# Performance work log

Hardware: AMD Instinct MI355X
Metric: run time of the kernel (lower is better)

## Reference

```python
import jax, jax.numpy as jnp
import numpy as np

DIM = 128
HEADS = 8
HD = DIM // HEADS          # 16
KS = 8                     # neighborhood kernel size
STRIDE = 2                 # GNA query-group stride
DIL = 2                    # dilation


def axis_indices(L, k, s, d):
    """Per-axis neighborhood indices [L, k] for dilated, strided, edge-clamped NA.

    Queries are grouped in blocks of `s`; every query in a block shares the
    window of the block's center query (GNA 'stride'). Dilation partitions the
    axis into `d` sub-grids; the window lives on the center query's sub-grid
    and is clamped so it never leaves the axis (natten-style sliding window).
    """
    idx = np.zeros((L, k), dtype=np.int32)
    for i in range(L):
        ic = min((i // s) * s + (s - 1) // 2, L - 1)   # group-center query
        r = ic % d                                      # sub-grid (residue)
        Lsub = (L - r + d - 1) // d                     # sub-grid length
        ii = ic // d                                    # index within sub-grid
        start = min(max(ii - (k - 1) // 2, 0), max(Lsub - k, 0))
        for j in range(k):
            idx[i, j] = r + d * min(start + j, Lsub - 1)
    return idx


def setup_inputs() -> dict:
    key = jax.random.key(0)
    ks = jax.random.split(key, 5)
    x = jax.random.normal(ks[0], (1, DIM, 96, 96), jnp.float32)
    # depthwise-grouped qkv conv: Conv2d(dim, 3*dim, 3, 1, 1, groups=dim)
    qkv_w = jax.random.normal(ks[1], (3 * DIM, 1, 3, 3), jnp.float32) * 0.1
    qkv_b = jax.random.normal(ks[2], (3 * DIM,), jnp.float32) * 0.02
    # 1x1 projection: Conv2d(dim, dim, 1)
    proj_w = jax.random.normal(ks[3], (DIM, DIM, 1, 1), jnp.float32) * (DIM ** -0.5)
    proj_b = jax.random.normal(ks[4], (DIM,), jnp.float32) * 0.02
    return {"x": x, "qkv_w": qkv_w, "qkv_b": qkv_b, "proj_w": proj_w, "proj_b": proj_b}


def reference(x, qkv_w, qkv_b, proj_w, proj_b):
    B, C, H, W = x.shape
    # grouped (groups=C) 3x3 conv producing q,k,v
    qkv = jax.lax.conv_general_dilated(
        x, qkv_w, window_strides=(1, 1), padding=[(1, 1), (1, 1)],
        dimension_numbers=("NCHW", "OIHW", "NCHW"), feature_group_count=C)
    qkv = qkv + qkv_b[None, :, None, None]
    qkv = qkv.reshape(B, 3, C, H, W)

    def to_heads(t):  # b c h w -> b h w nh hd
        return t.reshape(B, HEADS, HD, H, W).transpose(0, 3, 4, 1, 2)

    q = to_heads(qkv[:, 0])
    k = to_heads(qkv[:, 1])
    v = to_heads(qkv[:, 2])

    scale = HD ** -0.5
    ri = jnp.asarray(axis_indices(H, KS, STRIDE, DIL))  # [H, KS]
    ci = jnp.asarray(axis_indices(W, KS, STRIDE, DIL))  # [W, KS]
    R = ri[:, :, None, None]       # [H, KS, 1, 1]
    Cc = ci[None, None, :, :]      # [1, 1, W, KS]
    k_win = k[:, R, Cc]            # [B, H, KS, W, KS, nh, hd]
    v_win = v[:, R, Cc]

    logits = jnp.einsum("bijnd,bipjqnd->bijnpq", q * scale, k_win)
    attn = jax.nn.softmax(logits.reshape(B, H, W, HEADS, KS * KS), axis=-1)
    attn = attn.reshape(B, H, W, HEADS, KS, KS)
    out = jnp.einsum("bijnpq,bipjqnd->bijnd", attn, v_win)

    out = out.transpose(0, 3, 4, 1, 2).reshape(B, C, H, W)  # b h w nh hd -> b c h w
    out = jnp.einsum("bchw,oc->bohw", out, proj_w[:, :, 0, 0]) + proj_b[None, :, None, None]
    return out
```

## Files before the change

kernel.cpp:

```cpp
#include <hip/hip_runtime.h>
#include <hip/hip_bf16.h>

#define HH   96
#define WW   96
#define NPIX 9216
#define CH   128
#define NH   8
#define HD   16
#define KS   8

#define NEPIX   2304
#define NPOS    120
#define KVPITCH 40
#define QTPITCH 136
#define KVTPITCH 264
#define XPITCH  97

__device__ __forceinline__ unsigned short f2bf(float f) {
    __hip_bfloat16 b = __float2bfloat16(f);
    union { __hip_bfloat16 b; unsigned short u; } cv; cv.b = b; return cv.u;
}
__device__ __forceinline__ void u4_to_f8(uint4 u, float* f) {
    f[0] = __uint_as_float(u.x << 16); f[1] = __uint_as_float(u.x & 0xffff0000u);
    f[2] = __uint_as_float(u.y << 16); f[3] = __uint_as_float(u.y & 0xffff0000u);
    f[4] = __uint_as_float(u.z << 16); f[5] = __uint_as_float(u.z & 0xffff0000u);
    f[6] = __uint_as_float(u.w << 16); f[7] = __uint_as_float(u.w & 0xffff0000u);
}

__global__ __launch_bounds__(256) void conv_kernel(
    const float* __restrict__ x,
    const float* __restrict__ w,
    const float* __restrict__ bias,
    unsigned short* __restrict__ q_pm,
    unsigned short* __restrict__ kv_pm)
{
    __shared__ float ldsx[128 * XPITCH];
    __shared__ unsigned short qt [24 * QTPITCH];
    __shared__ unsigned short kvt[12 * KVTPITCH];

    const int row = blockIdx.x >> 2;
    const int qtr = blockIdx.x & 3;
    const int j0q = qtr * 24;
    const int tid = threadIdx.x;
    const int g   = tid >> 1;
    const int sh  = tid & 1;
    const bool kvrow = (row & 1) == 0;

    #pragma unroll
    for (int it = 0; it < 12; ++it) {
        const int t  = it * 256 + tid;
        const int r  = t >> 10;
        const int c  = (t >> 3) & 127;
        const int s4 = t & 7;
        const int rg = row + r - 1;
        const int j  = j0q - 4 + s4 * 4;
        float4 v = make_float4(0.f, 0.f, 0.f, 0.f);
        if (rg >= 0 && rg < HH && j >= 0 && j < WW)
            v = *(const float4*)(x + (size_t)c * NPIX + rg * WW + j);
        *(float4*)&ldsx[c * XPITCH + r * 32 + s4 * 4] = v;
    }
    __syncthreads();

    float xr[3][14];
    {
        const float* xg_l = &ldsx[g * XPITCH + 3 + sh * 12];
        #pragma unroll
        for (int dr = 0; dr < 3; ++dr)
            #pragma unroll
            for (int m = 0; m < 14; ++m)
                xr[dr][m] = xg_l[dr * 32 + m];
    }

    #pragma unroll
    for (int dt = 0; dt < 3; ++dt) {
        const int o = 3 * g + dt;
        const int t = o >> 7;
        const int c = o & 127;
        float w9[9];
        #pragma unroll
        for (int k = 0; k < 9; ++k) w9[k] = w[o * 9 + k];
        const float b = bias[o];

        if (t == 0) {
            #pragma unroll
            for (int px = 0; px < 12; ++px) {
                float acc = b;
                #pragma unroll
                for (int kh = 0; kh < 3; ++kh)
                    #pragma unroll
                    for (int kw = 0; kw < 3; ++kw)
                        acc += xr[kh][px + kw] * w9[kh * 3 + kw];
                qt[(sh * 12 + px) * QTPITCH + c] = f2bf(acc);
            }
        } else if (kvrow) {
            #pragma unroll
            for (int pe = 0; pe < 6; ++pe) {
                const int px = pe * 2;
                float acc = b;
                #pragma unroll
                for (int kh = 0; kh < 3; ++kh)
                    #pragma unroll
                    for (int kw = 0; kw < 3; ++kw)
                        acc += xr[kh][px + kw] * w9[kh * 3 + kw];
                kvt[(sh * 6 + pe) * KVTPITCH + (t - 1) * CH + c] = f2bf(acc);
            }
        }
    }

    __syncthreads();

    const int ntask = kvrow ? 768 : 384;
    #pragma unroll
    for (int it = 0; it < 3; ++it) {
        const int idx = it * 256 + tid;
        if (idx < 384) {
            const int px  = idx >> 4;
            const int c8  = (idx & 15) * 8;
            const uint4 v = *(const uint4*)&qt[px * QTPITCH + c8];
            *(uint4*)(q_pm + ((size_t)(row * WW) + j0q + px) * CH + c8) = v;
        } else if (idx < ntask) {
            const int k2  = idx - 384;
            const int epx = k2 >> 5;
            const int c32 = (k2 & 31) * 8;
            const int t1  = c32 >> 7;
            const int c   = c32 & 127;
            const uint4 v = *(const uint4*)&kvt[epx * KVTPITCH + c32];
            *(uint4*)(kv_pm + ((size_t)t1 * NEPIX + (row >> 1) * 48
                               + (j0q >> 1) + epx) * CH + c) = v;
        }
    }
}

__global__ __launch_bounds__(256) void attn_kernel(
    const unsigned short* __restrict__ q_pm,
    const unsigned short* __restrict__ kv_pm,
    float* __restrict__ a_t)
{
    __shared__ unsigned short kv[2][NPOS * KVPITCH];

    const int tid = threadIdx.x;
    const int seg = blockIdx.x;
    const int hp  = blockIdx.y;
    const int i   = seg / 6;
    const int j0  = (seg - i * 6) * 16;
    const int rs     = 2 * min(max(i / 2 - 3, 0), 40);
    const int cs_min = 2 * min(max(j0 / 2 - 3, 0), 40);
    const int er0 = rs >> 1;
    const int ec0 = cs_min >> 1;

    #pragma unroll
    for (int it = 0; it < 4; ++it) {
        const int idx = it * 256 + tid;
        if (idx < 960) {
            const int kvsel = idx / 480;
            const int rem   = idx - kvsel * 480;
            const int pos   = rem >> 2;
            const int sub   = rem & 3;
            const int p     = pos / 15;
            const int cc    = pos - p * 15;
            const int ec    = min(ec0 + cc, 47);
            const int ep    = (er0 + p) * 48 + ec;
            *(uint4*)&kv[kvsel][pos * KVPITCH + sub * 8] =
                *(const uint4*)(kv_pm + ((size_t)kvsel * NEPIX + ep) * CH
                                + hp * 32 + sub * 8);
        }
    }

    const int lane  = tid & 63;
    const int wave  = tid >> 6;
    const int r     = lane >> 3;
    const int hh    = (lane >> 2) & 1;
    const int px    = wave * 4 + (lane & 3);
    const int h     = hp * 2 + hh;
    const int pix   = seg * 16 + px;
    const int j     = j0 + px;
    const int ci0   = (2 * min(max(j / 2 - 3, 0), 40) - cs_min) >> 1;

    float qr[HD];
    {
        const unsigned short* qp = q_pm + (size_t)pix * CH + h * HD;
        u4_to_f8(*(const uint4*)qp, qr);
        u4_to_f8(*(const uint4*)(qp + 8), qr + 8);
        #pragma unroll
        for (int d = 0; d < HD; ++d) qr[d] *= 0.25f;
    }

    __syncthreads();

    const int posr = r * 15 + ci0;
    float lg[KS];
    float m = -1e30f;
    #pragma unroll
    for (int q = 0; q < KS; ++q) {
        const unsigned short* kp = &kv[0][(posr + q) * KVPITCH + hh * HD];
        float kf[HD];
        u4_to_f8(*(const uint4*)kp, kf);
        u4_to_f8(*(const uint4*)(kp + 8), kf + 8);
        float acc = 0.f;
        #pragma unroll
        for (int d = 0; d < HD; ++d) acc += qr[d] * kf[d];
        lg[q] = acc;
        m = fmaxf(m, acc);
    }

    float s = 0.f;
    #pragma unroll
    for (int q = 0; q < KS; ++q) { lg[q] = __expf(lg[q] - m); s += lg[q]; }

    float o[HD];
    #pragma unroll
    for (int d = 0; d < HD; ++d) o[d] = 0.f;
    #pragma unroll
    for (int q = 0; q < KS; ++q) {
        const unsigned short* vp = &kv[1][(posr + q) * KVPITCH + hh * HD];
        float vf[HD];
        u4_to_f8(*(const uint4*)vp, vf);
        u4_to_f8(*(const uint4*)(vp + 8), vf + 8);
        const float wgt = lg[q];
        #pragma unroll
        for (int d = 0; d < HD; ++d) o[d] += wgt * vf[d];
    }

    #pragma unroll
    for (int mask = 8; mask <= 32; mask <<= 1) {
        const float m2 = __shfl_xor(m, mask);
        const float s2 = __shfl_xor(s, mask);
        const float mn = fmaxf(m, m2);
        const float ea = __expf(m - mn);
        const float eb = __expf(m2 - mn);
        s = s * ea + s2 * eb;
        #pragma unroll
        for (int d = 0; d < HD; ++d) {
            const float o2 = __shfl_xor(o[d], mask);
            o[d] = o[d] * ea + o2 * eb;
        }
        m = mn;
    }
    const float inv = 1.f / s;

    a_t[(size_t)(h * HD + 2 * r)     * NPIX + pix] = o[2 * r]     * inv;
    a_t[(size_t)(h * HD + 2 * r + 1) * NPIX + pix] = o[2 * r + 1] * inv;
}

__global__ __launch_bounds__(256) void proj_kernel(
    const float* __restrict__ a_t,
    const float* __restrict__ pw,
    const float* __restrict__ pb,
    float* __restrict__ out)
{
    __shared__ float at[CH][36];

    const int tid = threadIdx.x;
    const int px0 = blockIdx.x * 32;

    #pragma unroll
    for (int it = 0; it < 4; ++it) {
        const int idx = it * 256 + tid;
        const int c   = idx >> 3;
        const int p4  = (idx & 7) * 4;
        *(float4*)&at[c][p4] =
            *(const float4*)(a_t + (size_t)c * NPIX + px0 + p4);
    }
    __syncthreads();

    const int og = tid >> 3;
    const int o0 = og * 4;
    const int p0 = (tid & 7) * 4;

    float acc[4][4];
    #pragma unroll
    for (int i = 0; i < 4; ++i) {
        const float b = pb[o0 + i];
        #pragma unroll
        for (int j = 0; j < 4; ++j) acc[i][j] = b;
    }

    #pragma unroll 2
    for (int c0 = 0; c0 < CH; c0 += 4) {
        float4 wv[4];
        #pragma unroll
        for (int i = 0; i < 4; ++i)
            wv[i] = *(const float4*)(pw + (size_t)(o0 + i) * CH + c0);
        float4 av[4];
        #pragma unroll
        for (int k = 0; k < 4; ++k)
            av[k] = *(const float4*)&at[c0 + k][p0];
        #pragma unroll
        for (int i = 0; i < 4; ++i) {
            acc[i][0] += wv[i].x * av[0].x; acc[i][1] += wv[i].x * av[0].y;
            acc[i][2] += wv[i].x * av[0].z; acc[i][3] += wv[i].x * av[0].w;
            acc[i][0] += wv[i].y * av[1].x; acc[i][1] += wv[i].y * av[1].y;
            acc[i][2] += wv[i].y * av[1].z; acc[i][3] += wv[i].y * av[1].w;
            acc[i][0] += wv[i].z * av[2].x; acc[i][1] += wv[i].z * av[2].y;
            acc[i][2] += wv[i].z * av[2].z; acc[i][3] += wv[i].z * av[2].w;
            acc[i][0] += wv[i].w * av[3].x; acc[i][1] += wv[i].w * av[3].y;
            acc[i][2] += wv[i].w * av[3].z; acc[i][3] += wv[i].w * av[3].w;
        }
    }

    #pragma unroll
    for (int i = 0; i < 4; ++i)
        *(float4*)(out + (size_t)(o0 + i) * NPIX + px0 + p0)
            = make_float4(acc[i][0], acc[i][1], acc[i][2], acc[i][3]);
}

extern "C" void kernel_launch(void* const* d_in, const int* in_sizes, int n_in,
                              void* d_out, int out_size, void* d_ws, size_t ws_size,
                              hipStream_t stream)
{
    const float* x      = (const float*)d_in[0];
    const float* qkv_w  = (const float*)d_in[1];
    const float* qkv_b  = (const float*)d_in[2];
    const float* proj_w = (const float*)d_in[3];
    const float* proj_b = (const float*)d_in[4];
    float* out = (float*)d_out;

    unsigned short* q_pm  = (unsigned short*)d_ws;
    unsigned short* kv_pm = q_pm + (size_t)NPIX * CH;
    float*          a_t   = (float*)(kv_pm + (size_t)2 * NEPIX * CH);

    conv_kernel<<<384, 256, 0, stream>>>(x, qkv_w, qkv_b, q_pm, kv_pm);
    attn_kernel<<<dim3(576, 4), 256, 0, stream>>>(q_pm, kv_pm, a_t);
    proj_kernel<<<288, 256, 0, stream>>>(a_t, proj_w, proj_b, out);
}
```

Baseline: 99.57 us.

## Fuse neighborhood attention and 1x1 projection into one 1024-thread kernel

Merges the attention and projection kernels. Each block now covers all four head pairs for a 16-pixel segment, loads the full 128-channel K/V tile into shared memory once, keeps the attention output in shared memory, and applies the 128x128 projection in place. This removes the a_t round trip through global memory and one kernel launch. In exchange, blocks become much larger with more shared memory, which lowers occupancy. The projection's register tiling is also much smaller, so each thread reads more weights from global or cache.

```diff
diff --git a/kernel.cpp b/kernel.cpp
--- a/kernel.cpp
+++ b/kernel.cpp
@@ -11,10 +11,11 @@
 
 #define NEPIX   2304
 #define NPOS    120
-#define KVPITCH 40
 #define QTPITCH 136
 #define KVTPITCH 264
 #define XPITCH  97
+#define KVP2    136
+#define AOPITCH 132
 
 __device__ __forceinline__ unsigned short f2bf(float f) {
     __hip_bfloat16 b = __float2bfloat16(f);
@@ -131,16 +132,18 @@
     }
 }
 
-__global__ __launch_bounds__(256) void attn_kernel(
+__global__ __launch_bounds__(1024) void attnproj_kernel(
     const unsigned short* __restrict__ q_pm,
     const unsigned short* __restrict__ kv_pm,
-    float* __restrict__ a_t)
+    const float* __restrict__ pw,
+    const float* __restrict__ pb,
+    float* __restrict__ out)
 {
-    __shared__ unsigned short kv[2][NPOS * KVPITCH];
+    __shared__ unsigned short kv[2][NPOS][KVP2];
+    __shared__ float ao[16][AOPITCH];
 
     const int tid = threadIdx.x;
     const int seg = blockIdx.x;
-    const int hp  = blockIdx.y;
     const int i   = seg / 6;
     const int j0  = (seg - i * 6) * 16;
     const int rs     = 2 * min(max(i / 2 - 3, 0), 40);
@@ -150,27 +153,28 @@
 
     #pragma unroll
     for (int it = 0; it < 4; ++it) {
-        const int idx = it * 256 + tid;
-        if (idx < 960) {
-            const int kvsel = idx / 480;
-            const int rem   = idx - kvsel * 480;
-            const int pos   = rem >> 2;
-            const int sub   = rem & 3;
+        const int idx = it * 1024 + tid;
+        if (idx < 3840) {
+            const int kvsel = idx / 1920;
+            const int rem   = idx - kvsel * 1920;
+            const int pos   = rem >> 4;
+            const int c8    = rem & 15;
             const int p     = pos / 15;
             const int cc    = pos - p * 15;
             const int ec    = min(ec0 + cc, 47);
             const int ep    = (er0 + p) * 48 + ec;
-            *(uint4*)&kv[kvsel][pos * KVPITCH + sub * 8] =
-                *(const uint4*)(kv_pm + ((size_t)kvsel * NEPIX + ep) * CH
-                                + hp * 32 + sub * 8);
-        }
-    }
-
-    const int lane  = tid & 63;
-    const int wave  = tid >> 6;
+            *(uint4*)&kv[kvsel][pos][c8 * 8] =
+                *(const uint4*)(kv_pm + ((size_t)kvsel * NEPIX + ep) * CH + c8 * 8);
+        }
+    }
+
+    const int hp    = tid >> 8;
+    const int t256  = tid & 255;
+    const int lane  = t256 & 63;
+    const int wv    = t256 >> 6;
     const int r     = lane >> 3;
     const int hh    = (lane >> 2) & 1;
-    const int px    = wave * 4 + (lane & 3);
+    const int px    = wv * 4 + (lane & 3);
     const int h     = hp * 2 + hh;
     const int pix   = seg * 16 + px;
     const int j     = j0 + px;
@@ -192,7 +196,7 @@
     float m = -1e30f;
     #pragma unroll
     for (int q = 0; q < KS; ++q) {
-        const unsigned short* kp = &kv[0][(posr + q) * KVPITCH + hh * HD];
+        const unsigned short* kp = &kv[0][posr + q][hp * 32 + hh * HD];
         float kf[HD];
         u4_to_f8(*(const uint4*)kp, kf);
         u4_to_f8(*(const uint4*)(kp + 8), kf + 8);
@@ -212,7 +216,7 @@
     for (int d = 0; d < HD; ++d) o[d] = 0.f;
     #pragma unroll
     for (int q = 0; q < KS; ++q) {
-        const unsigned short* vp = &kv[1][(posr + q) * KVPITCH + hh * HD];
+        const unsigned short* vp = &kv[1][posr + q][hp * 32 + hh * HD];
         float vf[HD];
         u4_to_f8(*(const uint4*)vp, vf);
         u4_to_f8(*(const uint4*)(vp + 8), vf + 8);
@@ -238,70 +242,31 @@
     }
     const float inv = 1.f / s;
 
-    a_t[(size_t)(h * HD + 2 * r)     * NPIX + pix] = o[2 * r]     * inv;
-    a_t[(size_t)(h * HD + 2 * r + 1) * NPIX + pix] = o[2 * r + 1] * inv;
-}
-
-__global__ __launch_bounds__(256) void proj_kernel(
-    const float* __restrict__ a_t,
-    const float* __restrict__ pw,
-    const float* __restrict__ pb,
-    float* __restrict__ out)
-{
-    __shared__ float at[CH][36];
-
-    const int tid = threadIdx.x;
-    const int px0 = blockIdx.x * 32;
-
-    #pragma unroll
-    for (int it = 0; it < 4; ++it) {
-        const int idx = it * 256 + tid;
-        const int c   = idx >> 3;
-        const int p4  = (idx & 7) * 4;
-        *(float4*)&at[c][p4] =
-            *(const float4*)(a_t + (size_t)c * NPIX + px0 + p4);
-    }
-    __syncthreads();
-
-    const int og = tid >> 3;
-    const int o0 = og * 4;
-    const int p0 = (tid & 7) * 4;
-
-    float acc[4][4];
-    #pragma unroll
-    for (int i = 0; i < 4; ++i) {
-        const float b = pb[o0 + i];
-        #pragma unroll
-        for (int j = 0; j < 4; ++j) acc[i][j] = b;
-    }
-
-    #pragma unroll 2
+    ao[px][h * HD + 2 * r]     = o[2 * r]     * inv;
+    ao[px][h * HD + 2 * r + 1] = o[2 * r + 1] * inv;
+
+    __syncthreads();
+
+    const int og  = tid >> 4;
+    const int o0  = og * 2;
+    const int ppx = tid & 15;
+
+    float acc0 = pb[o0];
+    float acc1 = pb[o0 + 1];
+    #pragma unroll 4
     for (int c0 = 0; c0 < CH; c0 += 4) {
-        float4 wv[4];
-        #pragma unroll
-        for (int i = 0; i < 4; ++i)
-            wv[i] = *(const float4*)(pw + (size_t)(o0 + i) * CH + c0);
-        float4 av[4];
-        #pragma unroll
-        for (int k = 0; k < 4; ++k)
-            av[k] = *(const float4*)&at[c0 + k][p0];
-        #pragma unroll
-        for (int i = 0; i < 4; ++i) {
-            acc[i][0] += wv[i].x * av[0].x; acc[i][1] += wv[i].x * av[0].y;
-            acc[i][2] += wv[i].x * av[0].z; acc[i][3] += wv[i].x * av[0].w;
-            acc[i][0] += wv[i].y * av[1].x; acc[i][1] += wv[i].y * av[1].y;
-            acc[i][2] += wv[i].y * av[1].z; acc[i][3] += wv[i].y * av[1].w;
-            acc[i][0] += wv[i].z * av[2].x; acc[i][1] += wv[i].z * av[2].y;
-            acc[i][2] += wv[i].z * av[2].z; acc[i][3] += wv[i].z * av[2].w;
-            acc[i][0] += wv[i].w * av[3].x; acc[i][1] += wv[i].w * av[3].y;
-            acc[i][2] += wv[i].w * av[3].z; acc[i][3] += wv[i].w * av[3].w;
-        }
-    }
-
-    #pragma unroll
-    for (int i = 0; i < 4; ++i)
-        *(float4*)(out + (size_t)(o0 + i) * NPIX + px0 + p0)
-            = make_float4(acc[i][0], acc[i][1], acc[i][2], acc[i][3]);
+        const float4 av = *(const float4*)&ao[ppx][c0];
+        const float4 w0 = *(const float4*)(pw + (size_t)o0 * CH + c0);
+        const float4 w1 = *(const float4*)(pw + (size_t)(o0 + 1) * CH + c0);
+        acc0 += av.x * w0.x; acc0 += av.y * w0.y;
+        acc0 += av.z * w0.z; acc0 += av.w * w0.w;
+        acc1 += av.x * w1.x; acc1 += av.y * w1.y;
+        acc1 += av.z * w1.z; acc1 += av.w * w1.w;
+    }
+
+    const int pxg = seg * 16 + ppx;
+    out[(size_t)o0 * NPIX + pxg]       = acc0;
+    out[(size_t)(o0 + 1) * NPIX + pxg] = acc1;
 }
 
 extern "C" void kernel_launch(void* const* d_in, const int* in_sizes, int n_in,
@@ -317,9 +282,7 @@
 
     unsigned short* q_pm  = (unsigned short*)d_ws;
     unsigned short* kv_pm = q_pm + (size_t)NPIX * CH;
-    float*          a_t   = (float*)(kv_pm + (size_t)2 * NEPIX * CH);
 
     conv_kernel<<<384, 256, 0, stream>>>(x, qkv_w, qkv_b, q_pm, kv_pm);
-    attn_kernel<<<dim3(576, 4), 256, 0, stream>>>(q_pm, kv_pm, a_t);
-    proj_kernel<<<288, 256, 0, stream>>>(a_t, proj_w, proj_b, out);
-}
+    attnproj_kernel<<<576, 1024, 0, stream>>>(q_pm, kv_pm, proj_w, proj_b, out);
+}
```

Result: slower. 116.5 us (+17.0%).

## Compute neighborhood attention with MFMA bf16 and transposed V layout

Applied to the files above, without the earlier changes.

Rewrites the attention kernel so QK^T and PV run as 16x16x32 bf16 MFMA tiles over a padded 8x16 window per query row, with an out-of-window mask. The conv kernel now writes K and a channel-major transposed V so V tiles load straight into MFMA operands. Probabilities are split into high and low bf16 parts to keep accuracy. One 512-thread block now covers all heads. This replaces scalar FMA loops and the LDS KV staging, at the cost of wasted MFMA work on masked columns and unaligned V shuffles.

```diff
diff --git a/kernel.cpp b/kernel.cpp
--- a/kernel.cpp
+++ b/kernel.cpp
@@ -10,21 +10,20 @@
 #define KS   8
 
 #define NEPIX   2304
-#define NPOS    120
-#define KVPITCH 40
 #define QTPITCH 136
 #define KVTPITCH 264
 #define XPITCH  97
+#define PPITCH  280
+
+typedef __attribute__((ext_vector_type(8))) short bf16x8;
+typedef __attribute__((ext_vector_type(4))) float f32x4;
 
 __device__ __forceinline__ unsigned short f2bf(float f) {
     __hip_bfloat16 b = __float2bfloat16(f);
     union { __hip_bfloat16 b; unsigned short u; } cv; cv.b = b; return cv.u;
 }
-__device__ __forceinline__ void u4_to_f8(uint4 u, float* f) {
-    f[0] = __uint_as_float(u.x << 16); f[1] = __uint_as_float(u.x & 0xffff0000u);
-    f[2] = __uint_as_float(u.y << 16); f[3] = __uint_as_float(u.y & 0xffff0000u);
-    f[4] = __uint_as_float(u.z << 16); f[5] = __uint_as_float(u.z & 0xffff0000u);
-    f[6] = __uint_as_float(u.w << 16); f[7] = __uint_as_float(u.w & 0xffff0000u);
+__device__ __forceinline__ bf16x8 u4_as_bf(uint4 u) {
+    union { uint4 u; bf16x8 b; } cv; cv.u = u; return cv.b;
 }
 
 __global__ __launch_bounds__(256) void conv_kernel(
@@ -32,7 +31,8 @@
     const float* __restrict__ w,
     const float* __restrict__ bias,
     unsigned short* __restrict__ q_pm,
-    unsigned short* __restrict__ kv_pm)
+    unsigned short* __restrict__ k_pm,
+    unsigned short* __restrict__ vt_pm)
 {
     __shared__ float ldsx[128 * XPITCH];
     __shared__ unsigned short qt [24 * QTPITCH];
@@ -53,10 +53,10 @@
         const int c  = (t >> 3) & 127;
         const int s4 = t & 7;
         const int rg = row + r - 1;
-        const int j  = j0q - 4 + s4 * 4;
+        const int jj = j0q - 4 + s4 * 4;
         float4 v = make_float4(0.f, 0.f, 0.f, 0.f);
-        if (rg >= 0 && rg < HH && j >= 0 && j < WW)
-            v = *(const float4*)(x + (size_t)c * NPIX + rg * WW + j);
+        if (rg >= 0 && rg < HH && jj >= 0 && jj < WW)
+            v = *(const float4*)(x + (size_t)c * NPIX + rg * WW + jj);
         *(float4*)&ldsx[c * XPITCH + r * 32 + s4 * 4] = v;
     }
     __syncthreads();
@@ -67,8 +67,8 @@
         #pragma unroll
         for (int dr = 0; dr < 3; ++dr)
             #pragma unroll
-            for (int m = 0; m < 14; ++m)
-                xr[dr][m] = xg_l[dr * 32 + m];
+            for (int mm = 0; mm < 14; ++mm)
+                xr[dr][mm] = xg_l[dr * 32 + mm];
     }
 
     #pragma unroll
@@ -109,137 +109,162 @@
 
     __syncthreads();
 
-    const int ntask = kvrow ? 768 : 384;
-    #pragma unroll
-    for (int it = 0; it < 3; ++it) {
+    const int ntask = kvrow ? 1088 : 384;
+    #pragma unroll
+    for (int it = 0; it < 5; ++it) {
         const int idx = it * 256 + tid;
         if (idx < 384) {
             const int px  = idx >> 4;
             const int c8  = (idx & 15) * 8;
             const uint4 v = *(const uint4*)&qt[px * QTPITCH + c8];
             *(uint4*)(q_pm + ((size_t)(row * WW) + j0q + px) * CH + c8) = v;
+        } else if (idx < 576 && kvrow) {
+            const int k2  = idx - 384;
+            const int epx = k2 >> 4;
+            const int c8  = (k2 & 15) * 8;
+            const uint4 v = *(const uint4*)&kvt[epx * KVTPITCH + c8];
+            *(uint4*)(k_pm + ((size_t)(row >> 1) * 48 + (j0q >> 1) + epx) * CH + c8) = v;
         } else if (idx < ntask) {
-            const int k2  = idx - 384;
-            const int epx = k2 >> 5;
-            const int c32 = (k2 & 31) * 8;
-            const int t1  = c32 >> 7;
-            const int c   = c32 & 127;
-            const uint4 v = *(const uint4*)&kvt[epx * KVTPITCH + c32];
-            *(uint4*)(kv_pm + ((size_t)t1 * NEPIX + (row >> 1) * 48
-                               + (j0q >> 1) + epx) * CH + c) = v;
-        }
-    }
-}
-
-__global__ __launch_bounds__(256) void attn_kernel(
+            const int v2   = idx - 576;
+            const int c    = v2 >> 2;
+            const int quad = v2 & 3;
+            if (quad < 3) {
+                const int e0 = quad * 4;
+                const unsigned short* src = &kvt[CH + c];
+                const unsigned int a0 =
+                    (unsigned int)src[(e0 + 0) * KVTPITCH]
+                    | ((unsigned int)src[(e0 + 1) * KVTPITCH] << 16);
+                const unsigned int a1 =
+                    (unsigned int)src[(e0 + 2) * KVTPITCH]
+                    | ((unsigned int)src[(e0 + 3) * KVTPITCH] << 16);
+                *(uint2*)(vt_pm + (size_t)c * NEPIX + (row >> 1) * 48
+                          + (j0q >> 1) + e0) = make_uint2(a0, a1);
+            }
+        }
+    }
+}
+
+__global__ __launch_bounds__(512, 4) void attn_kernel(
     const unsigned short* __restrict__ q_pm,
-    const unsigned short* __restrict__ kv_pm,
+    const unsigned short* __restrict__ k_pm,
+    const unsigned short* __restrict__ vt_pm,
     float* __restrict__ a_t)
 {
-    __shared__ unsigned short kv[2][NPOS * KVPITCH];
-
-    const int tid = threadIdx.x;
+    __shared__ unsigned short plds[NH][16 * PPITCH];
+
     const int seg = blockIdx.x;
-    const int hp  = blockIdx.y;
     const int i   = seg / 6;
     const int j0  = (seg - i * 6) * 16;
-    const int rs     = 2 * min(max(i / 2 - 3, 0), 40);
-    const int cs_min = 2 * min(max(j0 / 2 - 3, 0), 40);
-    const int er0 = rs >> 1;
-    const int ec0 = cs_min >> 1;
-
-    #pragma unroll
-    for (int it = 0; it < 4; ++it) {
-        const int idx = it * 256 + tid;
-        if (idx < 960) {
-            const int kvsel = idx / 480;
-            const int rem   = idx - kvsel * 480;
-            const int pos   = rem >> 2;
-            const int sub   = rem & 3;
-            const int p     = pos / 15;
-            const int cc    = pos - p * 15;
-            const int ec    = min(ec0 + cc, 47);
-            const int ep    = (er0 + p) * 48 + ec;
-            *(uint4*)&kv[kvsel][pos * KVPITCH + sub * 8] =
-                *(const uint4*)(kv_pm + ((size_t)kvsel * NEPIX + ep) * CH
-                                + hp * 32 + sub * 8);
-        }
-    }
-
-    const int lane  = tid & 63;
-    const int wave  = tid >> 6;
-    const int r     = lane >> 3;
-    const int hh    = (lane >> 2) & 1;
-    const int px    = wave * 4 + (lane & 3);
-    const int h     = hp * 2 + hh;
-    const int pix   = seg * 16 + px;
-    const int j     = j0 + px;
-    const int ci0   = (2 * min(max(j / 2 - 3, 0), 40) - cs_min) >> 1;
-
-    float qr[HD];
-    {
-        const unsigned short* qp = q_pm + (size_t)pix * CH + h * HD;
-        u4_to_f8(*(const uint4*)qp, qr);
-        u4_to_f8(*(const uint4*)(qp + 8), qr + 8);
-        #pragma unroll
-        for (int d = 0; d < HD; ++d) qr[d] *= 0.25f;
-    }
-
-    __syncthreads();
-
-    const int posr = r * 15 + ci0;
-    float lg[KS];
+    const int er0 = min(max(i / 2 - 3, 0), 40);
+    const int ec0 = min(max(j0 / 2 - 3, 0), 40);
+
+    const int tid  = threadIdx.x;
+    const int h    = tid >> 6;
+    const int lane = tid & 63;
+    const int nn   = lane & 15;
+    const int g    = lane >> 4;
+
+    const int j   = j0 + nn;
+    const int ci0 = min(max(j / 2 - 3, 0), 40) - ec0;
+
+    bf16x8 qf = (bf16x8)(short)0;
+    if (g < 2)
+        qf = u4_as_bf(*(const uint4*)(q_pm + (size_t)(seg * 16 + nn) * CH
+                                      + h * HD + g * 8));
+    const f32x4 zacc = {0.f, 0.f, 0.f, 0.f};
+    f32x4 st[8];
+    #pragma unroll
+    for (int t = 0; t < 8; ++t) {
+        bf16x8 kf = (bf16x8)(short)0;
+        if (g < 2) {
+            const int ep = (er0 + t) * 48 + min(ec0 + nn, 47);
+            kf = u4_as_bf(*(const uint4*)(k_pm + (size_t)ep * CH
+                                          + h * HD + g * 8));
+        }
+        st[t] = __builtin_amdgcn_mfma_f32_16x16x32_bf16(kf, qf, zacc, 0, 0, 0);
+    }
+
     float m = -1e30f;
     #pragma unroll
-    for (int q = 0; q < KS; ++q) {
-        const unsigned short* kp = &kv[0][(posr + q) * KVPITCH + hh * HD];
-        float kf[HD];
-        u4_to_f8(*(const uint4*)kp, kf);
-        u4_to_f8(*(const uint4*)(kp + 8), kf + 8);
-        float acc = 0.f;
-        #pragma unroll
-        for (int d = 0; d < HD; ++d) acc += qr[d] * kf[d];
-        lg[q] = acc;
-        m = fmaxf(m, acc);
-    }
+    for (int t = 0; t < 8; ++t)
+        #pragma unroll
+        for (int r = 0; r < 4; ++r) {
+            const int cc = g * 4 + r;
+            float T = st[t][r] * 0.25f;
+            T = ((unsigned)(cc - ci0) < 8u) ? T : -1e30f;
+            st[t][r] = T;
+            m = fmaxf(m, T);
+        }
+    m = fmaxf(m, __shfl_xor(m, 16));
+    m = fmaxf(m, __shfl_xor(m, 32));
 
     float s = 0.f;
     #pragma unroll
-    for (int q = 0; q < KS; ++q) { lg[q] = __expf(lg[q] - m); s += lg[q]; }
-
-    float o[HD];
-    #pragma unroll
-    for (int d = 0; d < HD; ++d) o[d] = 0.f;
-    #pragma unroll
-    for (int q = 0; q < KS; ++q) {
-        const unsigned short* vp = &kv[1][(posr + q) * KVPITCH + hh * HD];
-        float vf[HD];
-        u4_to_f8(*(const uint4*)vp, vf);
-        u4_to_f8(*(const uint4*)(vp + 8), vf + 8);
-        const float wgt = lg[q];
-        #pragma unroll
-        for (int d = 0; d < HD; ++d) o[d] += wgt * vf[d];
-    }
-
-    #pragma unroll
-    for (int mask = 8; mask <= 32; mask <<= 1) {
-        const float m2 = __shfl_xor(m, mask);
-        const float s2 = __shfl_xor(s, mask);
-        const float mn = fmaxf(m, m2);
-        const float ea = __expf(m - mn);
-        const float eb = __expf(m2 - mn);
-        s = s * ea + s2 * eb;
-        #pragma unroll
-        for (int d = 0; d < HD; ++d) {
-            const float o2 = __shfl_xor(o[d], mask);
-            o[d] = o[d] * ea + o2 * eb;
-        }
-        m = mn;
-    }
+    for (int t = 0; t < 8; ++t)
+        #pragma unroll
+        for (int r = 0; r < 4; ++r) {
+            const float p = __expf(st[t][r] - m);
+            st[t][r] = p;
+            s += p;
+        }
+    s += __shfl_xor(s, 16);
+    s += __shfl_xor(s, 32);
+
+    unsigned short* pl = &plds[h][nn * PPITCH];
+    const int g4 = g * 4;
+    #pragma unroll
+    for (int t = 0; t < 8; ++t) {
+        const float p0 = st[t][0], p1 = st[t][1], p2 = st[t][2], p3 = st[t][3];
+        const unsigned short h0 = f2bf(p0), h1 = f2bf(p1),
+                             h2 = f2bf(p2), h3 = f2bf(p3);
+        const float r0 = p0 - __uint_as_float((unsigned)h0 << 16);
+        const float r1 = p1 - __uint_as_float((unsigned)h1 << 16);
+        const float r2 = p2 - __uint_as_float((unsigned)h2 << 16);
+        const float r3 = p3 - __uint_as_float((unsigned)h3 << 16);
+        const unsigned short l0 = f2bf(r0), l1 = f2bf(r1),
+                             l2 = f2bf(r2), l3 = f2bf(r3);
+        *(uint2*)&pl[t * 16 + g4] =
+            make_uint2((unsigned)h0 | ((unsigned)h1 << 16),
+                       (unsigned)h2 | ((unsigned)h3 << 16));
+        *(uint2*)&pl[136 + t * 16 + g4] =
+            make_uint2((unsigned)l0 | ((unsigned)l1 << 16),
+                       (unsigned)l2 | ((unsigned)l3 << 16));
+    }
+
+    const unsigned short* vbase = vt_pm + (size_t)(h * HD + nn) * NEPIX;
+    const int ecs = ec0 & ~7;
+    const int shft = ec0 & 7;
+    f32x4 acc = {0.f, 0.f, 0.f, 0.f};
+    #pragma unroll
+    for (int kt = 0; kt < 4; ++kt) {
+        const int vrow = er0 + kt * 2 + (g >> 1);
+        const int coff = vrow * 48 + ecs + (g & 1) * 8;
+        const uint4 u0 = *(const uint4*)(vbase + coff);
+        bf16x8 vf;
+        if (shft == 0) {
+            vf = u4_as_bf(u0);
+        } else {
+            const uint4 u1 = *(const uint4*)(vbase + coff + 8);
+            const unsigned int s2 = u0.z, s3 = u0.w,
+                               s4 = u1.x, s5 = u1.y, s6 = u1.z;
+            uint4 o;
+            o.x = (s2 >> 16) | (s3 << 16);
+            o.y = (s3 >> 16) | (s4 << 16);
+            o.z = (s4 >> 16) | (s5 << 16);
+            o.w = (s5 >> 16) | (s6 << 16);
+            vf = u4_as_bf(o);
+        }
+        const bf16x8 ph = u4_as_bf(*(const uint4*)&pl[kt * 32 + g * 8]);
+        const bf16x8 po = u4_as_bf(*(const uint4*)&pl[136 + kt * 32 + g * 8]);
+        acc = __builtin_amdgcn_mfma_f32_16x16x32_bf16(vf, ph, acc, 0, 0, 0);
+        acc = __builtin_amdgcn_mfma_f32_16x16x32_bf16(vf, po, acc, 0, 0, 0);
+    }
+
     const float inv = 1.f / s;
-
-    a_t[(size_t)(h * HD + 2 * r)     * NPIX + pix] = o[2 * r]     * inv;
-    a_t[(size_t)(h * HD + 2 * r + 1) * NPIX + pix] = o[2 * r + 1] * inv;
+    const int pix = seg * 16 + nn;
+    #pragma unroll
+    for (int r = 0; r < 4; ++r)
+        a_t[(size_t)(h * HD + g4 + r) * NPIX + pix] = acc[r] * inv;
 }
 
 __global__ __launch_bounds__(256) void proj_kernel(
@@ -272,7 +297,7 @@
     for (int i = 0; i < 4; ++i) {
         const float b = pb[o0 + i];
         #pragma unroll
-        for (int j = 0; j < 4; ++j) acc[i][j] = b;
+        for (int jj = 0; jj < 4; ++jj) acc[i][jj] = b;
     }
 
     #pragma unroll 2
@@ -315,11 +340,12 @@
     const float* proj_b = (const float*)d_in[4];
     float* out = (float*)d_out;
 
-    unsigned short* q_pm  = (unsigned short*)d_ws;
-    unsigned short* kv_pm = q_pm + (size_t)NPIX * CH;
-    float*          a_t   = (float*)(kv_pm + (size_t)2 * NEPIX * CH);
-
-    conv_kernel<<<384, 256, 0, stream>>>(x, qkv_w, qkv_b, q_pm, kv_pm);
-    attn_kernel<<<dim3(576, 4), 256, 0, stream>>>(q_pm, kv_pm, a_t);
+    unsigned short* vt_pm = (unsigned short*)d_ws;
+    unsigned short* q_pm  = vt_pm + (size_t)CH * NEPIX;
+    unsigned short* k_pm  = q_pm + (size_t)NPIX * CH;
+    float*          a_t   = (float*)(k_pm + (size_t)NEPIX * CH);
+
+    conv_kernel<<<384, 256, 0, stream>>>(x, qkv_w, qkv_b, q_pm, k_pm, vt_pm);
+    attn_kernel<<<576, 512, 0, stream>>>(q_pm, k_pm, vt_pm, a_t);
     proj_kernel<<<288, 256, 0, stream>>>(a_t, proj_w, proj_b, out);
 }
```

New measurement: 95.92 us. -3.7%, faster.
